# Performance work log

Hardware: AMD Instinct MI355X
Metric: run time of the kernel (lower is better)

Reference implementation:

```python
import jax, jax.numpy as jnp
import numpy as np

N = 100000
E = 400000
NFEAT, NHID, NOUT, NHEAD = 128, 64, 128, 4
HIDDEN = NHID * NHEAD  # 256
SLOPE = 0.2


def gat_conv(x, src, dst, W, a_src, a_dst, b, concat):
    """PyG-style GATConv (eval mode, self-loops already appended to src/dst).
    x: [N, Fin]; W: [Fin, H*C]; a_src/a_dst: [H, C]; b: [H*C] or [C]."""
    H, C = a_src.shape
    h = (x @ W).reshape(N, H, C)                      # [N,H,C]
    al_s = (h * a_src).sum(-1)                        # [N,H] per-node src score
    al_d = (h * a_dst).sum(-1)                        # [N,H] per-node dst score
    e = jax.nn.leaky_relu(al_s[src] + al_d[dst], SLOPE)  # [Et,H]
    # segment softmax over incoming edges of each dst node
    m = jax.ops.segment_max(e, dst, num_segments=N)
    m = jnp.where(jnp.isfinite(m), m, 0.0)
    ex = jnp.exp(e - m[dst])
    denom = jax.ops.segment_sum(ex, dst, num_segments=N)
    alpha = ex / (denom[dst] + 1e-16)                 # [Et,H]
    msg = alpha[:, :, None] * h[src]                  # [Et,H,C]
    out = jax.ops.segment_sum(msg, dst, num_segments=N)  # [N,H,C]
    out = out.reshape(N, H * C) if concat else out.mean(axis=1)
    return out + b


def setup_inputs() -> dict:
    key = jax.random.key(0)
    ks = jax.random.split(key, 16)
    x = jax.random.normal(ks[0], (N, NFEAT), dtype=jnp.float32)
    edge_index = jax.random.randint(ks[1], (2, E), 0, N, dtype=jnp.int64)
    s = 0.1
    inp = {
        'x': x, 'edge_index': edge_index,
        # layer 0: nfeat -> nhid x nhead (concat)
        'W0': jax.random.normal(ks[2], (NFEAT, HIDDEN), jnp.float32) * s,
        'as0': jax.random.normal(ks[3], (NHEAD, NHID), jnp.float32) * s,
        'ad0': jax.random.normal(ks[4], (NHEAD, NHID), jnp.float32) * s,
        'b0': jnp.zeros((HIDDEN,), jnp.float32),
        # layer 1: hidden -> nhid x nhead (concat)
        'W1': jax.random.normal(ks[5], (HIDDEN, HIDDEN), jnp.float32) * s,
        'as1': jax.random.normal(ks[6], (NHEAD, NHID), jnp.float32) * s,
        'ad1': jax.random.normal(ks[7], (NHEAD, NHID), jnp.float32) * s,
        'b1': jnp.zeros((HIDDEN,), jnp.float32),
        # output layer: hidden -> nout, heads=1, concat=False
        'W2': jax.random.normal(ks[8], (HIDDEN, NOUT), jnp.float32) * s,
        'as2': jax.random.normal(ks[9], (1, NOUT), jnp.float32) * s,
        'ad2': jax.random.normal(ks[10], (1, NOUT), jnp.float32) * s,
        'b2': jnp.zeros((NOUT,), jnp.float32),
    }
    return inp


def reference(x, edge_index, W0, as0, ad0, b0, W1, as1, ad1, b1, W2, as2, ad2, b2):
    # PyG GATConv adds self-loops by default; edge set is shared across layers.
    loop = jnp.arange(N, dtype=edge_index.dtype)
    src = jnp.concatenate([edge_index[0], loop])
    dst = jnp.concatenate([edge_index[1], loop])
    # dropout inactive in eval mode
    h = jax.nn.elu(gat_conv(x, src, dst, W0, as0, ad0, b0, concat=True))
    h = jax.nn.elu(gat_conv(h, src, dst, W1, as1, ad1, b1, concat=True))
    out = gat_conv(h, src, dst, W2, as2, ad2, b2, concat=False)
    return out
```

## Files before the change

kernel.cpp:

```cpp
#include <hip/hip_runtime.h>
#include <cmath>

#define NN 100000
#define EE 400000
#define SLOPE 0.2f
#define MAXDEG 32

typedef __attribute__((ext_vector_type(8))) short short8;
typedef __attribute__((ext_vector_type(4))) float floatx4;

__device__ __forceinline__ float b2f(ushort u) {
    union { unsigned int i; float f; } v; v.i = ((unsigned int)u) << 16; return v.f;
}
__device__ __forceinline__ ushort f2b(float f) {
    union { float f; unsigned int i; } v; v.f = f;
    unsigned int r = v.i + 0x7FFFu + ((v.i >> 16) & 1u);
    return (ushort)(r >> 16);
}

__device__ __forceinline__ void gload16(const ushort* g, ushort* l) {
    __builtin_amdgcn_global_load_lds((const __attribute__((address_space(1))) void*)g,
                                     (__attribute__((address_space(3))) void*)l, 16, 0, 0);
}

__global__ __launch_bounds__(256) void prep(int* __restrict__ cnt,
                                            float* __restrict__ als2, float* __restrict__ ald2,
                                            const float* __restrict__ W0, const float* __restrict__ W1,
                                            const float* __restrict__ W2,
                                            ushort* __restrict__ Wt0, ushort* __restrict__ Wt1,
                                            ushort* __restrict__ Wt2) {
    int idx = blockIdx.x * 256 + threadIdx.x;
    if (idx < 25000) {
        ((int4*)cnt)[idx] = make_int4(0, 0, 0, 0);
    } else if (idx < 50000) {
        ((float4*)als2)[idx - 25000] = make_float4(0.f, 0.f, 0.f, 0.f);
    } else if (idx < 75000) {
        ((float4*)ald2)[idx - 50000] = make_float4(0.f, 0.f, 0.f, 0.f);
    } else {
        int j = idx - 75000;
        if (j < 32768) {
            int n = j >> 7, k = j & 127;
            Wt0[j] = f2b(W0[(size_t)k * 256 + n]);
        } else if (j < 98304) {
            int t = j - 32768;
            int n = t >> 8, k = t & 255;
            Wt1[t] = f2b(W1[(size_t)k * 256 + n]);
        } else if (j < 131072) {
            int t = j - 98304;
            int n = t >> 8, k = t & 255;
            Wt2[t] = f2b(W2[(size_t)k * 128 + n]);
        }
    }
}

__global__ __launch_bounds__(256) void bucket_scatter(const int* __restrict__ ei,
                                                      int* __restrict__ cnt,
                                                      int* __restrict__ bucket) {
    int e = blockIdx.x * 256 + threadIdx.x;
    if (e < EE) {
        int d = ei[EE + e];
        int p = atomicAdd(&cnt[d], 1);
        if (p < MAXDEG) bucket[(d << 5) + p] = ei[e];
    }
}

template <bool CVT, int BM, int BN, int KK>
__global__ __launch_bounds__(512) void gemm_bf16(const void* __restrict__ Avoid,
                                                 const ushort* __restrict__ Bt,
                                                 ushort* __restrict__ C,
                                                 int M,
                                                 const float* __restrict__ asf,
                                                 const float* __restrict__ adf,
                                                 float* __restrict__ als,
                                                 float* __restrict__ ald,
                                                 int H, int lgC) {
    constexpr int NSA = BM / 64;
    constexpr int NSB = BN / 64;
    constexpr int NCW = BN / 64;
    __shared__ __attribute__((aligned(16))) ushort As[BM * 64];
    __shared__ __attribute__((aligned(16))) ushort Bs[BN * 64];
    int tid = threadIdx.x;
    int wave = tid >> 6, lane = tid & 63;
    int wrow = wave / NCW, wcol = wave % NCW;
    int wm = wrow * 64, wn = wcol * 64;
    int bm = blockIdx.x * BM;

    floatx4 acc[4][4];
#pragma unroll
    for (int i = 0; i < 4; i++)
#pragma unroll
        for (int j = 0; j < 4; j++) acc[i][j] = (floatx4)0.f;

    int rsub = lane >> 3;
    int klog8 = ((lane & 7) ^ rsub) * 8;
    int frow = lane & 15;
    int q = lane >> 4;
    int f7 = frow & 7;

    const float*  Af = (const float*)Avoid;
    const ushort* Ab = (const ushort*)Avoid;

    for (int k0 = 0; k0 < KK; k0 += 64) {
        if constexpr (CVT) {
#pragma unroll
            for (int i = 0; i < NSA; i++) {
                int arow = bm + (wave + 8 * i) * 8 + rsub;
                float4 f0 = make_float4(0.f, 0.f, 0.f, 0.f), f1 = f0;
                if (arow < M) {
                    const float4* ap = (const float4*)(Af + (size_t)arow * KK + k0 + klog8);
                    f0 = ap[0]; f1 = ap[1];
                }
                uint4 pk;
                pk.x = (uint)f2b(f0.x) | ((uint)f2b(f0.y) << 16);
                pk.y = (uint)f2b(f0.z) | ((uint)f2b(f0.w) << 16);
                pk.z = (uint)f2b(f1.x) | ((uint)f2b(f1.y) << 16);
                pk.w = (uint)f2b(f1.z) | ((uint)f2b(f1.w) << 16);
                *(uint4*)&As[(wave + 8 * i) * 512 + lane * 8] = pk;
            }
        } else {
#pragma unroll
            for (int i = 0; i < NSA; i++)
                gload16(Ab + (size_t)(bm + (wave + 8 * i) * 8 + rsub) * KK + k0 + klog8,
                        &As[(wave + 8 * i) * 512]);
        }
#pragma unroll
        for (int i = 0; i < NSB; i++)
            gload16(Bt + (size_t)((wave + 8 * i) * 8 + rsub) * KK + k0 + klog8,
                    &Bs[(wave + 8 * i) * 512]);

        __syncthreads();

#pragma unroll
        for (int kk = 0; kk < 2; kk++) {
            short8 afr[4], bfr[4];
            int phys = ((kk * 4 + q) ^ f7) * 8;
#pragma unroll
            for (int i = 0; i < 4; i++)
                afr[i] = *(const short8*)&As[(wm + i * 16 + frow) * 64 + phys];
#pragma unroll
            for (int j = 0; j < 4; j++)
                bfr[j] = *(const short8*)&Bs[(wn + j * 16 + frow) * 64 + phys];
#pragma unroll
            for (int i = 0; i < 4; i++)
#pragma unroll
                for (int j = 0; j < 4; j++)
                    acc[i][j] = __builtin_amdgcn_mfma_f32_16x16x32_bf16(afr[i], bfr[j], acc[i][j], 0, 0, 0);
        }
        __syncthreads();
    }

    int ccol = wn + (lane & 15);
    int crow = bm + wm + (lane >> 4) * 4;
#pragma unroll
    for (int i = 0; i < 4; i++) {
#pragma unroll
        for (int reg = 0; reg < 4; reg++) {
            int row = crow + i * 16 + reg;
            if (row < M) {
#pragma unroll
                for (int j = 0; j < 4; j++)
                    C[(size_t)row * BN + ccol + j * 16] = f2b(acc[i][j][reg]);
            }
        }
    }

    {
        float asv[4], adv[4];
#pragma unroll
        for (int j = 0; j < 4; j++) {
            asv[j] = asf[wn + (lane & 15) + j * 16];
            adv[j] = adf[wn + (lane & 15) + j * 16];
        }
        int hidx = wn >> 6;
#pragma unroll
        for (int i = 0; i < 4; i++) {
#pragma unroll
            for (int reg = 0; reg < 4; reg++) {
                float ss = acc[i][0][reg] * asv[0] + acc[i][1][reg] * asv[1]
                         + acc[i][2][reg] * asv[2] + acc[i][3][reg] * asv[3];
                float dd = acc[i][0][reg] * adv[0] + acc[i][1][reg] * adv[1]
                         + acc[i][2][reg] * adv[2] + acc[i][3][reg] * adv[3];
#pragma unroll
                for (int off = 1; off < 16; off <<= 1) {
                    ss += __shfl_xor(ss, off, 64);
                    dd += __shfl_xor(dd, off, 64);
                }
                int row = crow + i * 16 + reg;
                if ((lane & 15) == 0 && row < M) {
                    if (lgC == 6) {
                        als[row * H + hidx] = ss;
                        ald[row * H + hidx] = dd;
                    } else {
                        atomicAdd(&als[row], ss);
                        atomicAdd(&ald[row], dd);
                    }
                }
            }
        }
    }
}

template <int H, int HC, bool ELU_ACT, bool OUT_BF16>
__global__ __launch_bounds__(256) void aggregate(const ushort* __restrict__ hlin,
                                                 const float* __restrict__ als,
                                                 const float* __restrict__ ald,
                                                 const int* __restrict__ cnt,
                                                 const int* __restrict__ bucket,
                                                 const float* __restrict__ bias,
                                                 void* __restrict__ outv) {
    constexpr int CP = HC / 64;
    constexpr int GS = 64 / H;
    int wv = threadIdx.x >> 6, lane = threadIdx.x & 63;
    int dst = blockIdx.x * 4 + wv;
    if (dst >= NN) return;
    int deg = min(cnt[dst], MAXDEG);
    int dtot = deg + 1;
    int rs = dst << 5;
    int eg = lane & (GS - 1);
    int head = lane / GS;
    float ad = ald[dst * H + head];

    float acc[CP];
#pragma unroll
    for (int j = 0; j < CP; j++) acc[j] = 0.f;

    uint laneoff = (uint)(lane * CP);

    if (dtot <= GS) {
        int src = 0;
        float s = -1e30f;
        if (eg < dtot) {
            src = (eg < deg) ? bucket[rs + eg] : dst;
            float sc = als[src * H + head] + ad;
            s = sc > 0.f ? sc : SLOPE * sc;
        }
        float m = s;
#pragma unroll
        for (int off = 1; off < GS; off <<= 1) m = fmaxf(m, __shfl_xor(m, off, 64));
        float e = (eg < dtot) ? __expf(s - m) : 0.f;
        float sum = e;
#pragma unroll
        for (int off = 1; off < GS; off <<= 1) sum += __shfl_xor(sum, off, 64);
        float w = e * (1.0f / (sum + 1e-16f));

        int hbase = head * GS;
        int d = 0;
        for (; d + 4 <= dtot; d += 4) {
            int s0 = __shfl(src, d, 64),     s1 = __shfl(src, d + 1, 64);
            int s2 = __shfl(src, d + 2, 64), s3 = __shfl(src, d + 3, 64);
            float w0 = __shfl(w, hbase + d, 64),     w1 = __shfl(w, hbase + d + 1, 64);
            float w2 = __shfl(w, hbase + d + 2, 64), w3 = __shfl(w, hbase + d + 3, 64);
            const uint* p0 = (const uint*)(hlin + (uint)s0 * HC + laneoff);
            const uint* p1 = (const uint*)(hlin + (uint)s1 * HC + laneoff);
            const uint* p2 = (const uint*)(hlin + (uint)s2 * HC + laneoff);
            const uint* p3 = (const uint*)(hlin + (uint)s3 * HC + laneoff);
            uint u0[CP / 2], u1[CP / 2], u2[CP / 2], u3[CP / 2];
#pragma unroll
            for (int qq = 0; qq < CP / 2; qq++) { u0[qq] = p0[qq]; u1[qq] = p1[qq]; u2[qq] = p2[qq]; u3[qq] = p3[qq]; }
#pragma unroll
            for (int qq = 0; qq < CP / 2; qq++) {
                acc[2*qq]   += w0 * b2f((ushort)(u0[qq] & 0xffff)) + w1 * b2f((ushort)(u1[qq] & 0xffff))
                             + w2 * b2f((ushort)(u2[qq] & 0xffff)) + w3 * b2f((ushort)(u3[qq] & 0xffff));
                acc[2*qq+1] += w0 * b2f((ushort)(u0[qq] >> 16)) + w1 * b2f((ushort)(u1[qq] >> 16))
                             + w2 * b2f((ushort)(u2[qq] >> 16)) + w3 * b2f((ushort)(u3[qq] >> 16));
            }
        }
        for (; d < dtot; d++) {
            int sd = __shfl(src, d, 64);
            float wd = __shfl(w, hbase + d, 64);
            const uint* p = (const uint*)(hlin + (uint)sd * HC + laneoff);
#pragma unroll
            for (int qq = 0; qq < CP / 2; qq++) {
                uint u = p[qq];
                acc[2*qq]   += wd * b2f((ushort)(u & 0xffff));
                acc[2*qq+1] += wd * b2f((ushort)(u >> 16));
            }
        }
    } else {
        float m = -1e30f;
        for (int e2 = eg; e2 < dtot; e2 += GS) {
            int s0 = (e2 < deg) ? bucket[rs + e2] : dst;
            float sc = als[s0 * H + head] + ad;
            sc = sc > 0.f ? sc : SLOPE * sc;
            m = fmaxf(m, sc);
        }
#pragma unroll
        for (int off = 1; off < GS; off <<= 1) m = fmaxf(m, __shfl_xor(m, off, 64));
        float sum = 0.f;
        for (int e2 = eg; e2 < dtot; e2 += GS) {
            int s0 = (e2 < deg) ? bucket[rs + e2] : dst;
            float sc = als[s0 * H + head] + ad;
            sc = sc > 0.f ? sc : SLOPE * sc;
            sum += __expf(sc - m);
        }
#pragma unroll
        for (int off = 1; off < GS; off <<= 1) sum += __shfl_xor(sum, off, 64);
        float inv = 1.0f / (sum + 1e-16f);
        for (int d = 0; d < dtot; d++) {
            int sd = (d < deg) ? bucket[rs + d] : dst;
            float sc = als[sd * H + head] + ad;
            sc = sc > 0.f ? sc : SLOPE * sc;
            float wd = __expf(sc - m) * inv;
            const uint* p = (const uint*)(hlin + (uint)sd * HC + laneoff);
#pragma unroll
            for (int qq = 0; qq < CP / 2; qq++) {
                uint u = p[qq];
                acc[2*qq]   += wd * b2f((ushort)(u & 0xffff));
                acc[2*qq+1] += wd * b2f((ushort)(u >> 16));
            }
        }
    }

#pragma unroll
    for (int j = 0; j < CP; j++) {
        float v = acc[j] + bias[lane * CP + j];
        if (ELU_ACT) v = v > 0.f ? v : (__expf(v) - 1.0f);
        acc[j] = v;
    }
    if (OUT_BF16) {
        ushort* outp = (ushort*)outv + (size_t)dst * HC + laneoff;
        uint pk[CP / 2];
#pragma unroll
        for (int qq = 0; qq < CP / 2; qq++)
            pk[qq] = (uint)f2b(acc[2*qq]) | ((uint)f2b(acc[2*qq+1]) << 16);
#pragma unroll
        for (int qq = 0; qq < CP / 2; qq++) ((uint*)outp)[qq] = pk[qq];
    } else {
        float* outp = (float*)outv + (size_t)dst * HC + laneoff;
#pragma unroll
        for (int j = 0; j < CP; j++) outp[j] = acc[j];
    }
}

extern "C" void kernel_launch(void* const* d_in, const int* in_sizes, int n_in,
                              void* d_out, int out_size, void* d_ws, size_t ws_size,
                              hipStream_t stream) {
    const float* x   = (const float*)d_in[0];
    const int*   ei  = (const int*)d_in[1];
    const float* W0  = (const float*)d_in[2];
    const float* as0 = (const float*)d_in[3];
    const float* ad0 = (const float*)d_in[4];
    const float* b0  = (const float*)d_in[5];
    const float* W1  = (const float*)d_in[6];
    const float* as1 = (const float*)d_in[7];
    const float* ad1 = (const float*)d_in[8];
    const float* b1  = (const float*)d_in[9];
    const float* W2  = (const float*)d_in[10];
    const float* as2 = (const float*)d_in[11];
    const float* ad2 = (const float*)d_in[12];
    const float* b2  = (const float*)d_in[13];
    float* out = (float*)d_out;

    char* ws = (char*)d_ws;
    size_t off = 0;
    auto alloc = [&](size_t bytes) {
        void* p = ws + off;
        off += (bytes + 255) & ~(size_t)255;
        return p;
    };
    ushort* h    = (ushort*)alloc((size_t)NN * 256 * 2);
    ushort* actB = (ushort*)alloc((size_t)(NN + 256) * 256 * 2);
    ushort* actC = (ushort*)alloc((size_t)(NN + 256) * 256 * 2);
    ushort* Wt0  = (ushort*)alloc((size_t)256 * 128 * 2);
    ushort* Wt1  = (ushort*)alloc((size_t)256 * 256 * 2);
    ushort* Wt2  = (ushort*)alloc((size_t)128 * 256 * 2);
    float* als   = (float*)alloc((size_t)NN * 4 * 4);
    float* ald   = (float*)alloc((size_t)NN * 4 * 4);
    float* als2  = (float*)alloc((size_t)NN * 4);
    float* ald2  = (float*)alloc((size_t)NN * 4);
    int* cnt     = (int*)alloc((size_t)NN * 4);
    int* bucket  = (int*)alloc((size_t)NN * MAXDEG * 4);

    prep<<<(75000 + 131072 + 255) / 256, 256, 0, stream>>>(cnt, als2, ald2, W0, W1, W2, Wt0, Wt1, Wt2);

    bucket_scatter<<<(EE + 255) / 256, 256, 0, stream>>>(ei, cnt, bucket);

    const int GM128 = (NN + 127) / 128;
    const int GM256 = (NN + 255) / 256;
    const int NB4 = (NN + 3) / 4;

    gemm_bf16<true, 128, 256, 128><<<GM128, 512, 0, stream>>>(x, Wt0, h, NN, as0, ad0, als, ald, 4, 6);
    aggregate<4, 256, true, true><<<NB4, 256, 0, stream>>>(h, als, ald, cnt, bucket, b0, actB);

    gemm_bf16<false, 128, 256, 256><<<GM128, 512, 0, stream>>>(actB, Wt1, h, NN, as1, ad1, als, ald, 4, 6);
    aggregate<4, 256, true, true><<<NB4, 256, 0, stream>>>(h, als, ald, cnt, bucket, b1, actC);

    gemm_bf16<false, 256, 128, 256><<<GM256, 512, 0, stream>>>(actC, Wt2, h, NN, as2, ad2, als2, ald2, 1, 7);
    aggregate<1, 128, false, false><<<NB4, 256, 0, stream>>>(h, als2, ald2, cnt, bucket, b2, out);
}
```

Baseline: 412.8 us.

## Replace LDS-tiled GEMM with persistent register-resident weight GEMM

Each wave now keeps a 64-column slab of the transposed weight matrix in registers for the whole run and loops persistently over 16-row chunks. A fragments are loaded straight from global memory, so LDS staging, global_load_lds and block barriers go away. The attention score reduction is fused per chunk as before. This removes shared-memory traffic and synchronization, but the A rows are read once per slab (4x or 2x redundant global reads), and register pressure from holding B fragments goes up.

Measured after the change: 415.2 us. About the same (+0.6%).

```diff
diff --git a/kernel.cpp b/kernel.cpp
--- a/kernel.cpp
+++ b/kernel.cpp
@@ -16,11 +16,6 @@
     union { float f; unsigned int i; } v; v.f = f;
     unsigned int r = v.i + 0x7FFFu + ((v.i >> 16) & 1u);
     return (ushort)(r >> 16);
-}
-
-__device__ __forceinline__ void gload16(const ushort* g, ushort* l) {
-    __builtin_amdgcn_global_load_lds((const __attribute__((address_space(1))) void*)g,
-                                     (__attribute__((address_space(3))) void*)l, 16, 0, 0);
 }
 
 __global__ __launch_bounds__(256) void prep(int* __restrict__ cnt,
@@ -64,136 +59,101 @@
     }
 }
 
-template <bool CVT, int BM, int BN, int KK>
-__global__ __launch_bounds__(512) void gemm_bf16(const void* __restrict__ Avoid,
-                                                 const ushort* __restrict__ Bt,
-                                                 ushort* __restrict__ C,
-                                                 int M,
-                                                 const float* __restrict__ asf,
-                                                 const float* __restrict__ adf,
-                                                 float* __restrict__ als,
-                                                 float* __restrict__ ald,
-                                                 int H, int lgC) {
-    constexpr int NSA = BM / 64;
-    constexpr int NSB = BN / 64;
-    constexpr int NCW = BN / 64;
-    __shared__ __attribute__((aligned(16))) ushort As[BM * 64];
-    __shared__ __attribute__((aligned(16))) ushort Bs[BN * 64];
-    int tid = threadIdx.x;
-    int wave = tid >> 6, lane = tid & 63;
-    int wrow = wave / NCW, wcol = wave % NCW;
-    int wm = wrow * 64, wn = wcol * 64;
-    int bm = blockIdx.x * BM;
-
-    floatx4 acc[4][4];
-#pragma unroll
-    for (int i = 0; i < 4; i++)
-#pragma unroll
-        for (int j = 0; j < 4; j++) acc[i][j] = (floatx4)0.f;
-
-    int rsub = lane >> 3;
-    int klog8 = ((lane & 7) ^ rsub) * 8;
+template <bool CVT, int KK, int NSLAB>
+__global__ __launch_bounds__(256) void gemm_reg(const void* __restrict__ Avoid,
+                                                const ushort* __restrict__ Bt,
+                                                ushort* __restrict__ C,
+                                                const float* __restrict__ asf,
+                                                const float* __restrict__ adf,
+                                                float* __restrict__ als,
+                                                float* __restrict__ ald,
+                                                int H, int lgC) {
+    constexpr int NK = KK / 32;
+    constexpr int NTOT = NSLAB * 64;
+    int tid  = threadIdx.x;
+    int lane = tid & 63;
+    int w    = blockIdx.x * 4 + (tid >> 6);
+    int slab = w & (NSLAB - 1);
+    int wst  = w / NSLAB;
+    int nwv  = (gridDim.x * 4) / NSLAB;
     int frow = lane & 15;
-    int q = lane >> 4;
-    int f7 = frow & 7;
+    int kq   = (lane >> 4) * 8;
+    int n0   = slab * 64;
+
+    short8 bfr[NK][4];
+#pragma unroll
+    for (int kk = 0; kk < NK; kk++)
+#pragma unroll
+        for (int j = 0; j < 4; j++)
+            bfr[kk][j] = *(const short8*)(Bt + (size_t)(n0 + j * 16 + frow) * KK + kk * 32 + kq);
+
+    float asv[4], adv[4];
+#pragma unroll
+    for (int j = 0; j < 4; j++) {
+        asv[j] = asf[n0 + j * 16 + frow];
+        adv[j] = adf[n0 + j * 16 + frow];
+    }
 
     const float*  Af = (const float*)Avoid;
     const ushort* Ab = (const ushort*)Avoid;
 
-    for (int k0 = 0; k0 < KK; k0 += 64) {
+    for (int c = wst; c < NN / 16; c += nwv) {
+        int r0 = c * 16;
+
+        short8 afr[NK];
         if constexpr (CVT) {
 #pragma unroll
-            for (int i = 0; i < NSA; i++) {
-                int arow = bm + (wave + 8 * i) * 8 + rsub;
-                float4 f0 = make_float4(0.f, 0.f, 0.f, 0.f), f1 = f0;
-                if (arow < M) {
-                    const float4* ap = (const float4*)(Af + (size_t)arow * KK + k0 + klog8);
-                    f0 = ap[0]; f1 = ap[1];
-                }
+            for (int kk = 0; kk < NK; kk++) {
+                const float4* ap = (const float4*)(Af + (size_t)(r0 + frow) * KK + kk * 32 + kq);
+                float4 f0 = ap[0], f1 = ap[1];
                 uint4 pk;
                 pk.x = (uint)f2b(f0.x) | ((uint)f2b(f0.y) << 16);
                 pk.y = (uint)f2b(f0.z) | ((uint)f2b(f0.w) << 16);
                 pk.z = (uint)f2b(f1.x) | ((uint)f2b(f1.y) << 16);
                 pk.w = (uint)f2b(f1.z) | ((uint)f2b(f1.w) << 16);
-                *(uint4*)&As[(wave + 8 * i) * 512 + lane * 8] = pk;
+                afr[kk] = *(short8*)&pk;
             }
         } else {
 #pragma unroll
-            for (int i = 0; i < NSA; i++)
-                gload16(Ab + (size_t)(bm + (wave + 8 * i) * 8 + rsub) * KK + k0 + klog8,
-                        &As[(wave + 8 * i) * 512]);
-        }
-#pragma unroll
-        for (int i = 0; i < NSB; i++)
-            gload16(Bt + (size_t)((wave + 8 * i) * 8 + rsub) * KK + k0 + klog8,
-                    &Bs[(wave + 8 * i) * 512]);
-
-        __syncthreads();
-
-#pragma unroll
-        for (int kk = 0; kk < 2; kk++) {
-            short8 afr[4], bfr[4];
-            int phys = ((kk * 4 + q) ^ f7) * 8;
-#pragma unroll
-            for (int i = 0; i < 4; i++)
-                afr[i] = *(const short8*)&As[(wm + i * 16 + frow) * 64 + phys];
+            for (int kk = 0; kk < NK; kk++)
+                afr[kk] = *(const short8*)(Ab + (size_t)(r0 + frow) * KK + kk * 32 + kq);
+        }
+
+        floatx4 acc[4];
+#pragma unroll
+        for (int j = 0; j < 4; j++) acc[j] = (floatx4)0.f;
+#pragma unroll
+        for (int kk = 0; kk < NK; kk++)
 #pragma unroll
             for (int j = 0; j < 4; j++)
-                bfr[j] = *(const short8*)&Bs[(wn + j * 16 + frow) * 64 + phys];
-#pragma unroll
-            for (int i = 0; i < 4; i++)
-#pragma unroll
-                for (int j = 0; j < 4; j++)
-                    acc[i][j] = __builtin_amdgcn_mfma_f32_16x16x32_bf16(afr[i], bfr[j], acc[i][j], 0, 0, 0);
-        }
-        __syncthreads();
-    }
-
-    int ccol = wn + (lane & 15);
-    int crow = bm + wm + (lane >> 4) * 4;
-#pragma unroll
-    for (int i = 0; i < 4; i++) {
+                acc[j] = __builtin_amdgcn_mfma_f32_16x16x32_bf16(afr[kk], bfr[kk][j], acc[j], 0, 0, 0);
+
+        int crow = r0 + (lane >> 4) * 4;
+#pragma unroll
+        for (int j = 0; j < 4; j++)
+#pragma unroll
+            for (int reg = 0; reg < 4; reg++)
+                C[(size_t)(crow + reg) * NTOT + n0 + j * 16 + frow] = f2b(acc[j][reg]);
+
 #pragma unroll
         for (int reg = 0; reg < 4; reg++) {
-            int row = crow + i * 16 + reg;
-            if (row < M) {
-#pragma unroll
-                for (int j = 0; j < 4; j++)
-                    C[(size_t)row * BN + ccol + j * 16] = f2b(acc[i][j][reg]);
-            }
-        }
-    }
-
-    {
-        float asv[4], adv[4];
-#pragma unroll
-        for (int j = 0; j < 4; j++) {
-            asv[j] = asf[wn + (lane & 15) + j * 16];
-            adv[j] = adf[wn + (lane & 15) + j * 16];
-        }
-        int hidx = wn >> 6;
-#pragma unroll
-        for (int i = 0; i < 4; i++) {
-#pragma unroll
-            for (int reg = 0; reg < 4; reg++) {
-                float ss = acc[i][0][reg] * asv[0] + acc[i][1][reg] * asv[1]
-                         + acc[i][2][reg] * asv[2] + acc[i][3][reg] * asv[3];
-                float dd = acc[i][0][reg] * adv[0] + acc[i][1][reg] * adv[1]
-                         + acc[i][2][reg] * adv[2] + acc[i][3][reg] * adv[3];
-#pragma unroll
-                for (int off = 1; off < 16; off <<= 1) {
-                    ss += __shfl_xor(ss, off, 64);
-                    dd += __shfl_xor(dd, off, 64);
-                }
-                int row = crow + i * 16 + reg;
-                if ((lane & 15) == 0 && row < M) {
-                    if (lgC == 6) {
-                        als[row * H + hidx] = ss;
-                        ald[row * H + hidx] = dd;
-                    } else {
-                        atomicAdd(&als[row], ss);
-                        atomicAdd(&ald[row], dd);
-                    }
+            float ss = acc[0][reg] * asv[0] + acc[1][reg] * asv[1]
+                     + acc[2][reg] * asv[2] + acc[3][reg] * asv[3];
+            float dd = acc[0][reg] * adv[0] + acc[1][reg] * adv[1]
+                     + acc[2][reg] * adv[2] + acc[3][reg] * adv[3];
+#pragma unroll
+            for (int off = 1; off < 16; off <<= 1) {
+                ss += __shfl_xor(ss, off, 64);
+                dd += __shfl_xor(dd, off, 64);
+            }
+            if (frow == 0) {
+                int row = crow + reg;
+                if (lgC == 6) {
+                    als[row * H + slab] = ss;
+                    ald[row * H + slab] = dd;
+                } else {
+                    atomicAdd(&als[row], ss);
+                    atomicAdd(&ald[row], dd);
                 }
             }
         }
@@ -359,8 +319,8 @@
         return p;
     };
     ushort* h    = (ushort*)alloc((size_t)NN * 256 * 2);
-    ushort* actB = (ushort*)alloc((size_t)(NN + 256) * 256 * 2);
-    ushort* actC = (ushort*)alloc((size_t)(NN + 256) * 256 * 2);
+    ushort* actB = (ushort*)alloc((size_t)NN * 256 * 2);
+    ushort* actC = (ushort*)alloc((size_t)NN * 256 * 2);
     ushort* Wt0  = (ushort*)alloc((size_t)256 * 128 * 2);
     ushort* Wt1  = (ushort*)alloc((size_t)256 * 256 * 2);
     ushort* Wt2  = (ushort*)alloc((size_t)128 * 256 * 2);
@@ -375,16 +335,14 @@
 
     bucket_scatter<<<(EE + 255) / 256, 256, 0, stream>>>(ei, cnt, bucket);
 
-    const int GM128 = (NN + 127) / 128;
-    const int GM256 = (NN + 255) / 256;
     const int NB4 = (NN + 3) / 4;
 
-    gemm_bf16<true, 128, 256, 128><<<GM128, 512, 0, stream>>>(x, Wt0, h, NN, as0, ad0, als, ald, 4, 6);
+    gemm_reg<true, 128, 4><<<512, 256, 0, stream>>>(x, Wt0, h, as0, ad0, als, ald, 4, 6);
     aggregate<4, 256, true, true><<<NB4, 256, 0, stream>>>(h, als, ald, cnt, bucket, b0, actB);
 
-    gemm_bf16<false, 128, 256, 256><<<GM128, 512, 0, stream>>>(actB, Wt1, h, NN, as1, ad1, als, ald, 4, 6);
+    gemm_reg<false, 256, 4><<<512, 256, 0, stream>>>(actB, Wt1, h, as1, ad1, als, ald, 4, 6);
     aggregate<4, 256, true, true><<<NB4, 256, 0, stream>>>(h, als, ald, cnt, bucket, b1, actC);
 
-    gemm_bf16<false, 256, 128, 256><<<GM256, 512, 0, stream>>>(actC, Wt2, h, NN, as2, ad2, als2, ald2, 1, 7);
+    gemm_reg<false, 256, 2><<<512, 256, 0, stream>>>(actC, Wt2, h, as2, ad2, als2, ald2, 1, 7);
     aggregate<1, 128, false, false><<<NB4, 256, 0, stream>>>(h, als2, ald2, cnt, bucket, b2, out);
 }
```
